# Kernel tuning notes

Measured on AMD Instinct MI355X. Metric: run time of the kernel, lower is better.

Reference implementation:

```python
import jax, jax.numpy as jnp
import numpy as np

N_NODES = 50000
N_EDGES = 1600000
D_IN = 128
D_OUT = 32
ALPHA = 0.2  # LeakyReLU negative slope


def setup_inputs() -> dict:
    key = jax.random.key(0)
    k1, k2, k3, k4, k5, k6 = jax.random.split(key, 6)
    gain = float(np.sqrt(2.0))  # relu gain, xavier_normal-style scale
    X = jax.random.normal(k1, (N_NODES, D_IN), dtype=jnp.float32)
    weights = jax.random.normal(k2, (D_IN, D_OUT), dtype=jnp.float32) * (gain * np.sqrt(2.0 / (D_IN + D_OUT)))
    a0 = jax.random.normal(k3, (1, D_OUT), dtype=jnp.float32) * (gain * np.sqrt(2.0 / (1 + D_OUT)))
    a1 = jax.random.normal(k4, (1, D_OUT), dtype=jnp.float32) * (gain * np.sqrt(2.0 / (1 + D_OUT)))
    row_idx = jax.random.randint(k5, (N_EDGES,), 0, N_NODES, dtype=jnp.int32)
    col_idx = jax.random.randint(k6, (N_EDGES,), 0, N_NODES, dtype=jnp.int32)
    return {"X": X, "weights": weights, "a0": a0, "a1": a1,
            "row_idx": row_idx, "col_idx": col_idx}


def _minmax_norm(v):
    vmin = jnp.min(v)
    vmax = jnp.max(v)
    return (v - vmin) / (vmax - vmin)


def reference(X, weights, a0, a1, row_idx, col_idx):
    # X_prime = X @ W  -> [N, D]
    X_prime = X @ weights
    # Per-node partial scores; edge score e(i->j) = a0.X_prime[i] + a1.X_prime[j]
    s0 = jnp.sum(X_prime * a0, axis=-1)  # [N]
    s1 = jnp.sum(X_prime * a1, axis=-1)  # [N]
    att = s0[row_idx] + s1[col_idx]      # [E]
    # leakyrelu -> min-max normalize over all edges -> exp
    att = jax.nn.leaky_relu(att, negative_slope=ALPHA)
    att = jnp.exp(_minmax_norm(att))
    # rows_sum = SpMM(att, ones) = per-destination-row sum of edge weights
    rows_sum = jax.ops.segment_sum(att, row_idx, num_segments=N_NODES)  # [N]
    # h_prime = SpMM(att, X_prime) / rows_sum  (dropout p=0 -> identity)
    h = jax.ops.segment_sum(att[:, None] * X_prime[col_idx], row_idx,
                            num_segments=N_NODES)  # [N, D]
    return h / rows_sum[:, None]
```

## Files before the change

kernel.cpp:

```cpp
#include <hip/hip_runtime.h>
#include <hip/hip_bf16.h>
#include <math.h>

#define N_NODES 50000
#define N_EDGES 1600000
#define D_IN 128
#define D_OUT 32
#define ALPHA 0.2f

#define NB   256
#define RPB  196
#define CAP  8192
#define HRPB 49
#define CAPH 2048
#define GST  16
#define PT   16
#define PBK  256
#define EB   (PT * PBK)
#define NEB  ((N_EDGES + EB - 1) / EB)
#define XNPB 32
#define NXB  ((N_NODES + XNPB - 1) / XNPB)
#define XLS  33

__device__ __forceinline__ int enc_f(float x) {
    int i = __float_as_int(x);
    return i >= 0 ? i : (i ^ 0x7fffffff);
}
__device__ __forceinline__ float dec_f(int k) {
    return __int_as_float(k >= 0 ? k : (k ^ 0x7fffffff));
}
__device__ __forceinline__ unsigned short f2bf(float x) {
    __hip_bfloat16 h = __float2bfloat16(x);
    return *(unsigned short*)&h;
}
__device__ __forceinline__ float bf2f(unsigned short u) {
    return __uint_as_float((unsigned)u << 16);
}

__global__ __launch_bounds__(256) void k_gemm(const float* __restrict__ X,
                                              const float* __restrict__ W,
                                              const float* __restrict__ a0,
                                              const float* __restrict__ a1,
                                              unsigned short* __restrict__ Xpb,
                                              float* __restrict__ s0,
                                              float* __restrict__ s1,
                                              int* __restrict__ gcount) {
    __shared__ float4 Wl4[1024];
    __shared__ float4 Xl4[XNPB * XLS];
    const int tid = threadIdx.x;
    if (blockIdx.x == 0) {
        int4* g4 = (int4*)gcount;
#pragma unroll
        for (int i = 0; i < NB * GST / 4 / 256; ++i)
            g4[tid + 256 * i] = make_int4(0, 0, 0, 0);
    }
    const int node0 = blockIdx.x * XNPB;
    {
        const float4* W4 = (const float4*)W;
#pragma unroll
        for (int i = 0; i < 4; ++i) Wl4[tid + 256 * i] = W4[tid + 256 * i];
        const float4* X4 = (const float4*)X + (size_t)node0 * (D_IN / 4);
        const int lim = (min(XNPB, N_NODES - node0)) * (D_IN / 4);
#pragma unroll
        for (int i = 0; i < 4; ++i) {
            const int idx = tid + 256 * i;
            const float4 v = (idx < lim) ? X4[idx]
                                         : make_float4(0.f, 0.f, 0.f, 0.f);
            Xl4[(idx >> 5) * XLS + (idx & 31)] = v;
        }
    }
    __syncthreads();
    const int g = tid >> 3;
    const int l = tid & 7;
    const int node = node0 + g;
    const float4* xr = &Xl4[g * XLS];
    float ax = 0.f, ay = 0.f, az = 0.f, aw = 0.f;
#pragma unroll 4
    for (int kk = 0; kk < D_IN / 4; ++kk) {
        const float4 xv = xr[kk];
        const float4 w0 = Wl4[(4 * kk + 0) * 8 + l];
        const float4 w1 = Wl4[(4 * kk + 1) * 8 + l];
        const float4 w2 = Wl4[(4 * kk + 2) * 8 + l];
        const float4 w3 = Wl4[(4 * kk + 3) * 8 + l];
        ax += xv.x * w0.x + xv.y * w1.x + xv.z * w2.x + xv.w * w3.x;
        ay += xv.x * w0.y + xv.y * w1.y + xv.z * w2.y + xv.w * w3.y;
        az += xv.x * w0.z + xv.y * w1.z + xv.z * w2.z + xv.w * w3.z;
        aw += xv.x * w0.w + xv.y * w1.w + xv.z * w2.w + xv.w * w3.w;
    }
    if (node < N_NODES) {
        uint2 pk;
        pk.x = ((unsigned)f2bf(ay) << 16) | f2bf(ax);
        pk.y = ((unsigned)f2bf(aw) << 16) | f2bf(az);
        ((uint2*)Xpb)[(size_t)node * 8 + l] = pk;
        const float4 av0 = ((const float4*)a0)[l];
        const float4 av1 = ((const float4*)a1)[l];
        float v0 = ax * av0.x + ay * av0.y + az * av0.z + aw * av0.w;
        float v1 = ax * av1.x + ay * av1.y + az * av1.z + aw * av1.w;
#pragma unroll
        for (int m = 4; m >= 1; m >>= 1) {
            v0 += __shfl_xor(v0, m);
            v1 += __shfl_xor(v1, m);
        }
        if (l == 0) { s0[node] = v0; s1[node] = v1; }
    }
}

__global__ __launch_bounds__(256) void k_edge(const int* __restrict__ row,
                                              const int* __restrict__ col,
                                              const float* __restrict__ s0,
                                              const float* __restrict__ s1,
                                              int* __restrict__ gcount,
                                              int2* __restrict__ mm,
                                              uint2* __restrict__ gEdges) {
    __shared__ int hist[NB];
    __shared__ int lcur[NB];
    __shared__ int smn[4], smx[4];
    const int tid = threadIdx.x;
    if (tid < NB) hist[tid] = 0;
    __syncthreads();
    const int base = blockIdx.x * EB;
    unsigned px[PT];
    float    fa[PT];
    int cnt = 0;
    int kmin = 0x7fffffff, kmax = 0x80000000;
    if (base + EB <= N_EDGES) {
#pragma unroll
        for (int i = 0; i < PT / 4; ++i) {
            const int4 r4 = ((const int4*)(row + base))[tid + i * PBK];
            const int4 c4 = ((const int4*)(col + base))[tid + i * PBK];
            const int rr[4] = {r4.x, r4.y, r4.z, r4.w};
            const int cc[4] = {c4.x, c4.y, c4.z, c4.w};
#pragma unroll
            for (int j = 0; j < 4; ++j) {
                const int r = rr[j];
                const int c = cc[j];
                float a = s0[r] + s1[c];
                a = a > 0.f ? a : ALPHA * a;
                const int k = enc_f(a);
                kmin = min(kmin, k);
                kmax = max(kmax, k);
                const unsigned b = (unsigned)r / RPB;
                const unsigned lr = (unsigned)r - b * RPB;
                px[cnt] = (b << 24) | (lr << 16) | (unsigned)c;
                fa[cnt] = a;
                ++cnt;
                atomicAdd(&hist[b], 1);
            }
        }
    } else {
#pragma unroll
        for (int i = 0; i < PT; ++i) {
            const int e = base + i * PBK + tid;
            if (e >= N_EDGES) break;
            const int r = row[e];
            const int c = col[e];
            float a = s0[r] + s1[c];
            a = a > 0.f ? a : ALPHA * a;
            const int k = enc_f(a);
            kmin = min(kmin, k);
            kmax = max(kmax, k);
            const unsigned b = (unsigned)r / RPB;
            const unsigned lr = (unsigned)r - b * RPB;
            px[cnt] = (b << 24) | (lr << 16) | (unsigned)c;
            fa[cnt] = a;
            ++cnt;
            atomicAdd(&hist[b], 1);
        }
    }
    __syncthreads();
    if (tid < NB) {
        const int h = hist[tid];
        lcur[tid] = h > 0 ? atomicAdd(&gcount[tid << 4], h) : 0;
    }
    __syncthreads();
    for (int j = 0; j < cnt; ++j) {
        const unsigned p = px[j];
        const unsigned b = p >> 24;
        const int pos = atomicAdd(&lcur[b], 1);
        if (pos < CAP)
            gEdges[(size_t)b * CAP + pos] =
                make_uint2(p, (unsigned)__float_as_int(fa[j]));
    }
#pragma unroll
    for (int m = 32; m >= 1; m >>= 1) {
        kmin = min(kmin, __shfl_xor(kmin, m));
        kmax = max(kmax, __shfl_xor(kmax, m));
    }
    const int wave = tid >> 6;
    if ((tid & 63) == 0) { smn[wave] = kmin; smx[wave] = kmax; }
    __syncthreads();
    if (tid == 0) {
#pragma unroll
        for (int w = 1; w < 4; ++w) {
            kmin = min(kmin, smn[w]);
            kmax = max(kmax, smx[w]);
        }
        mm[blockIdx.x] = make_int2(kmin, kmax);
    }
}

__global__ __launch_bounds__(512, 8) void k_bucket(const int* __restrict__ gcount,
                                                   const uint2* __restrict__ gEdges,
                                                   const unsigned short* __restrict__ Xpb,
                                                   const int2* __restrict__ mm,
                                                   float* __restrict__ out) {
    __shared__ unsigned short scol[CAPH];
    __shared__ float swt[CAPH];
    __shared__ int off[HRPB + 1];
    __shared__ int cur[HRPB];
    __shared__ int rmn[8], rmx[8];
    __shared__ float s_mn, s_inv;
    const int bid = blockIdx.x;
    const int b = bid >> 2;
    const int lo = (bid & 3) * HRPB;
    const int t = threadIdx.x;
    const int cnt = min(gcount[b << 4], CAP);
    const uint2* eb = gEdges + (size_t)b * CAP;

    int kmn = 0x7fffffff, kmx = 0x80000000;
    for (int i = t; i < NEB; i += 512) {
        const int2 v = mm[i];
        kmn = min(kmn, v.x);
        kmx = max(kmx, v.y);
    }
#pragma unroll
    for (int m = 32; m >= 1; m >>= 1) {
        kmn = min(kmn, __shfl_xor(kmn, m));
        kmx = max(kmx, __shfl_xor(kmx, m));
    }
    if ((t & 63) == 0) { rmn[t >> 6] = kmn; rmx[t >> 6] = kmx; }
    if (t < HRPB) cur[t] = 0;
    __syncthreads();
    if (t == 0) {
#pragma unroll
        for (int w = 1; w < 8; ++w) {
            kmn = min(kmn, rmn[w]);
            kmx = max(kmx, rmx[w]);
        }
        const float mn = dec_f(kmn);
        const float mx = dec_f(kmx);
        s_mn = mn;
        s_inv = 1.0f / (mx - mn);
    }
    for (int i = t; i < cnt; i += 512) {
        const int lrl = (int)((eb[i].x >> 16) & 0xFFu) - lo;
        if ((unsigned)lrl < (unsigned)HRPB) atomicAdd(&cur[lrl], 1);
    }
    __syncthreads();
    if (t == 0) {
        int run = 0;
#pragma unroll
        for (int r = 0; r < HRPB; ++r) { off[r] = run; run += cur[r]; }
        off[HRPB] = run;
    }
    __syncthreads();
    if (t < HRPB) cur[t] = off[t];
    __syncthreads();
    const float mn = s_mn;
    const float inv = s_inv;
    for (int i = t; i < cnt; i += 512) {
        const uint2 e = eb[i];
        const int lrl = (int)((e.x >> 16) & 0xFFu) - lo;
        if ((unsigned)lrl < (unsigned)HRPB) {
            const int p = atomicAdd(&cur[lrl], 1);
            if (p < CAPH) {
                scol[p] = (unsigned short)(e.x & 0xFFFFu);
                swt[p] = __expf((__int_as_float(e.y) - mn) * inv);
            }
        }
    }
    __syncthreads();

    const int proc = t >> 4;
    const int d2 = t & 15;
    const unsigned* Xp32 = (const unsigned*)Xpb;
    for (int lr = proc; lr < HRPB; lr += 32) {
        const int s = off[lr];
        const int e2 = min(off[lr + 1], CAPH);
        float pa0 = 0.f, pa1 = 0.f, pa2 = 0.f, pa3 = 0.f;
        float pb0 = 0.f, pb1 = 0.f, pb2 = 0.f, pb3 = 0.f;
        float w0s = 0.f, w1s = 0.f, w2s = 0.f, w3s = 0.f;
        int i = s;
        for (; i + 3 < e2; i += 4) {
            const int c0 = scol[i];
            const int c1 = scol[i + 1];
            const int c2 = scol[i + 2];
            const int c3 = scol[i + 3];
            const float w0 = swt[i];
            const float w1 = swt[i + 1];
            const float w2 = swt[i + 2];
            const float w3 = swt[i + 3];
            const unsigned u0 = Xp32[(size_t)c0 * 16 + d2];
            const unsigned u1 = Xp32[(size_t)c1 * 16 + d2];
            const unsigned u2 = Xp32[(size_t)c2 * 16 + d2];
            const unsigned u3 = Xp32[(size_t)c3 * 16 + d2];
            pa0 += w0 * bf2f((unsigned short)(u0 & 0xFFFFu));
            pb0 += w0 * bf2f((unsigned short)(u0 >> 16));
            pa1 += w1 * bf2f((unsigned short)(u1 & 0xFFFFu));
            pb1 += w1 * bf2f((unsigned short)(u1 >> 16));
            pa2 += w2 * bf2f((unsigned short)(u2 & 0xFFFFu));
            pb2 += w2 * bf2f((unsigned short)(u2 >> 16));
            pa3 += w3 * bf2f((unsigned short)(u3 & 0xFFFFu));
            pb3 += w3 * bf2f((unsigned short)(u3 >> 16));
            w0s += w0; w1s += w1; w2s += w2; w3s += w3;
        }
        for (; i < e2; ++i) {
            const float w = swt[i];
            const unsigned u = Xp32[(size_t)scol[i] * 16 + d2];
            pa0 += w * bf2f((unsigned short)(u & 0xFFFFu));
            pb0 += w * bf2f((unsigned short)(u >> 16));
            w0s += w;
        }
        const int r = b * RPB + lo + lr;
        if (r < N_NODES) {
            const float ws = w0s + w1s + w2s + w3s;
            float2 o;
            o.x = (pa0 + pa1 + pa2 + pa3) / ws;
            o.y = (pb0 + pb1 + pb2 + pb3) / ws;
            ((float2*)out)[(size_t)r * 16 + d2] = o;
        }
    }
}

extern "C" void kernel_launch(void* const* d_in, const int* in_sizes, int n_in,
                              void* d_out, int out_size, void* d_ws, size_t ws_size,
                              hipStream_t stream) {
    const float* X  = (const float*)d_in[0];
    const float* W  = (const float*)d_in[1];
    const float* a0 = (const float*)d_in[2];
    const float* a1 = (const float*)d_in[3];
    const int* row  = (const int*)d_in[4];
    const int* col  = (const int*)d_in[5];
    float* out = (float*)d_out;

    float* ws = (float*)d_ws;
    int*   gcount = (int*)ws + 64;
    int2*  mm = (int2*)((int*)ws + 64 + NB * GST);
    float* s0 = ws + 64 + NB * GST + 1024;
    float* s1 = s0 + 50048;
    unsigned short* Xpb = (unsigned short*)(s1 + 50048);
    uint2* gEdges = (uint2*)(s1 + 50048 + 800000);

    k_gemm<<<NXB, 256, 0, stream>>>(X, W, a0, a1, Xpb, s0, s1, gcount);
    k_edge<<<NEB, 256, 0, stream>>>(row, col, s0, s1, gcount, mm, gEdges);
    k_bucket<<<NB * 4, 512, 0, stream>>>(gcount, gEdges, Xpb, mm, out);
}
```

Baseline: 150.8 us.

## Stage edge records in LDS for coalesced bucket writes; one block per bucket

```diff
diff --git a/kernel.cpp b/kernel.cpp
--- a/kernel.cpp
+++ b/kernel.cpp
@@ -11,8 +11,6 @@
 #define NB   256
 #define RPB  196
 #define CAP  8192
-#define HRPB 49
-#define CAPH 2048
 #define GST  16
 #define PT   16
 #define PBK  256
@@ -112,8 +110,11 @@
                                               int* __restrict__ gcount,
                                               int2* __restrict__ mm,
                                               uint2* __restrict__ gEdges) {
+    __shared__ uint2 rec[EB];
     __shared__ int hist[NB];
+    __shared__ int off[NB + 1];
     __shared__ int lcur[NB];
+    __shared__ int gbase[NB];
     __shared__ int smn[4], smx[4];
     const int tid = threadIdx.x;
     if (tid < NB) hist[tid] = 0;
@@ -170,16 +171,28 @@
     __syncthreads();
     if (tid < NB) {
         const int h = hist[tid];
-        lcur[tid] = h > 0 ? atomicAdd(&gcount[tid << 4], h) : 0;
-    }
+        gbase[tid] = h > 0 ? atomicAdd(&gcount[tid << 4], h) : 0;
+    }
+    if (tid == 0) {
+        int run = 0;
+        for (int i = 0; i < NB; ++i) { off[i] = run; run += hist[i]; }
+        off[NB] = run;
+    }
+    __syncthreads();
+    if (tid < NB) lcur[tid] = off[tid];
     __syncthreads();
     for (int j = 0; j < cnt; ++j) {
-        const unsigned p = px[j];
-        const unsigned b = p >> 24;
-        const int pos = atomicAdd(&lcur[b], 1);
-        if (pos < CAP)
-            gEdges[(size_t)b * CAP + pos] =
-                make_uint2(p, (unsigned)__float_as_int(fa[j]));
+        const unsigned b = px[j] >> 24;
+        const int p = atomicAdd(&lcur[b], 1);
+        rec[p] = make_uint2(px[j], (unsigned)__float_as_int(fa[j]));
+    }
+    __syncthreads();
+    const int total = off[NB];
+    for (int i = tid; i < total; i += PBK) {
+        const uint2 e = rec[i];
+        const unsigned b = e.x >> 24;
+        const int pos = gbase[b] + (i - off[b]);
+        if (pos < CAP) gEdges[(size_t)b * CAP + pos] = e;
     }
 #pragma unroll
     for (int m = 32; m >= 1; m >>= 1) {
@@ -199,26 +212,24 @@
     }
 }
 
-__global__ __launch_bounds__(512, 8) void k_bucket(const int* __restrict__ gcount,
-                                                   const uint2* __restrict__ gEdges,
-                                                   const unsigned short* __restrict__ Xpb,
-                                                   const int2* __restrict__ mm,
-                                                   float* __restrict__ out) {
-    __shared__ unsigned short scol[CAPH];
-    __shared__ float swt[CAPH];
-    __shared__ int off[HRPB + 1];
-    __shared__ int cur[HRPB];
-    __shared__ int rmn[8], rmx[8];
+__global__ __launch_bounds__(1024, 1) void k_bucket(const int* __restrict__ gcount,
+                                                    const uint2* __restrict__ gEdges,
+                                                    const unsigned short* __restrict__ Xpb,
+                                                    const int2* __restrict__ mm,
+                                                    float* __restrict__ out) {
+    __shared__ unsigned short scol[CAP];
+    __shared__ float swt[CAP];
+    __shared__ int off[RPB + 1];
+    __shared__ int cur[RPB];
+    __shared__ int rmn[16], rmx[16];
     __shared__ float s_mn, s_inv;
-    const int bid = blockIdx.x;
-    const int b = bid >> 2;
-    const int lo = (bid & 3) * HRPB;
+    const int b = blockIdx.x;
     const int t = threadIdx.x;
     const int cnt = min(gcount[b << 4], CAP);
     const uint2* eb = gEdges + (size_t)b * CAP;
 
     int kmn = 0x7fffffff, kmx = 0x80000000;
-    for (int i = t; i < NEB; i += 512) {
+    for (int i = t; i < NEB; i += 1024) {
         const int2 v = mm[i];
         kmn = min(kmn, v.x);
         kmx = max(kmx, v.y);
@@ -229,11 +240,11 @@
         kmx = max(kmx, __shfl_xor(kmx, m));
     }
     if ((t & 63) == 0) { rmn[t >> 6] = kmn; rmx[t >> 6] = kmx; }
-    if (t < HRPB) cur[t] = 0;
+    if (t < RPB) cur[t] = 0;
     __syncthreads();
     if (t == 0) {
 #pragma unroll
-        for (int w = 1; w < 8; ++w) {
+        for (int w = 1; w < 16; ++w) {
             kmn = min(kmn, rmn[w]);
             kmx = max(kmx, rmx[w]);
         }
@@ -242,31 +253,27 @@
         s_mn = mn;
         s_inv = 1.0f / (mx - mn);
     }
-    for (int i = t; i < cnt; i += 512) {
-        const int lrl = (int)((eb[i].x >> 16) & 0xFFu) - lo;
-        if ((unsigned)lrl < (unsigned)HRPB) atomicAdd(&cur[lrl], 1);
-    }
+    for (int i = t; i < cnt; i += 1024)
+        atomicAdd(&cur[(eb[i].x >> 16) & 0xFFu], 1);
     __syncthreads();
     if (t == 0) {
         int run = 0;
 #pragma unroll
-        for (int r = 0; r < HRPB; ++r) { off[r] = run; run += cur[r]; }
-        off[HRPB] = run;
-    }
-    __syncthreads();
-    if (t < HRPB) cur[t] = off[t];
+        for (int r = 0; r < RPB; ++r) { off[r] = run; run += cur[r]; }
+        off[RPB] = run;
+    }
+    __syncthreads();
+    if (t < RPB) cur[t] = off[t];
     __syncthreads();
     const float mn = s_mn;
     const float inv = s_inv;
-    for (int i = t; i < cnt; i += 512) {
+    for (int i = t; i < cnt; i += 1024) {
         const uint2 e = eb[i];
-        const int lrl = (int)((e.x >> 16) & 0xFFu) - lo;
-        if ((unsigned)lrl < (unsigned)HRPB) {
-            const int p = atomicAdd(&cur[lrl], 1);
-            if (p < CAPH) {
-                scol[p] = (unsigned short)(e.x & 0xFFFFu);
-                swt[p] = __expf((__int_as_float(e.y) - mn) * inv);
-            }
+        const int lr = (int)((e.x >> 16) & 0xFFu);
+        const int p = atomicAdd(&cur[lr], 1);
+        if (p < CAP) {
+            scol[p] = (unsigned short)(e.x & 0xFFFFu);
+            swt[p] = __expf((__int_as_float(e.y) - mn) * inv);
         }
     }
     __syncthreads();
@@ -274,9 +281,9 @@
     const int proc = t >> 4;
     const int d2 = t & 15;
     const unsigned* Xp32 = (const unsigned*)Xpb;
-    for (int lr = proc; lr < HRPB; lr += 32) {
+    for (int lr = proc; lr < RPB; lr += 64) {
         const int s = off[lr];
-        const int e2 = min(off[lr + 1], CAPH);
+        const int e2 = off[lr + 1];
         float pa0 = 0.f, pa1 = 0.f, pa2 = 0.f, pa3 = 0.f;
         float pb0 = 0.f, pb1 = 0.f, pb2 = 0.f, pb3 = 0.f;
         float w0s = 0.f, w1s = 0.f, w2s = 0.f, w3s = 0.f;
@@ -311,7 +318,7 @@
             pb0 += w * bf2f((unsigned short)(u >> 16));
             w0s += w;
         }
-        const int r = b * RPB + lo + lr;
+        const int r = b * RPB + lr;
         if (r < N_NODES) {
             const float ws = w0s + w1s + w2s + w3s;
             float2 o;
@@ -343,5 +350,5 @@
 
     k_gemm<<<NXB, 256, 0, stream>>>(X, W, a0, a1, Xpb, s0, s1, gcount);
     k_edge<<<NEB, 256, 0, stream>>>(row, col, s0, s1, gcount, mm, gEdges);
-    k_bucket<<<NB * 4, 512, 0, stream>>>(gcount, gEdges, Xpb, mm, out);
-}
+    k_bucket<<<NB, 1024, 0, stream>>>(gcount, gEdges, Xpb, mm, out);
+}
```

Measured after the change: 144.2 us. -4.4%, faster.
